# Kernel tuning notes

Measured on AMD Instinct MI355X. Metric: run time of the kernel, lower is better.

## Reference

```python
import jax, jax.numpy as jnp
import numpy as np

B, S, HID = 2, 1024, 2048
H, KV, D = 32, 8, 64          # heads, kv heads, head_dim
G = H // KV                    # GQA groups
THETA = 10000.0


def _rope_cos_sin(seq_len):
    # (S, D/2) cos/sin tables, interleaved-pair RoPE
    freqs = 1.0 / THETA ** (jnp.arange(0, D, 2, dtype=jnp.float32) / D)
    t = jnp.arange(seq_len, dtype=jnp.float32)
    f = jnp.outer(t, freqs)
    return jnp.cos(f), jnp.sin(f)


def _apply_rope(x, cos, sin):
    # x: (B, S, h, D); cos/sin: (S, D/2) -> broadcast (1, S, 1, D/2)
    c = cos[None, :, None, :]
    s = sin[None, :, None, :]
    xe, xo = x[..., ::2], x[..., 1::2]
    oe = xe * c - xo * s
    oo = xo * c + xe * s
    # re-interleave even/odd
    return jnp.stack([oe, oo], axis=-1).reshape(x.shape)


def setup_inputs() -> dict:
    key = jax.random.key(0)
    ks = jax.random.split(key, 5)
    return {
        "hidden_states": jax.random.normal(ks[0], (B, S, HID), jnp.float32),
        "Wq": jax.random.normal(ks[1], (HID, H * D), jnp.float32) * 0.02,
        "Wk": jax.random.normal(ks[2], (HID, KV * D), jnp.float32) * 0.02,
        "Wv": jax.random.normal(ks[3], (HID, KV * D), jnp.float32) * 0.02,
        "Wo": jax.random.normal(ks[4], (H * D, HID), jnp.float32) * 0.02,
    }


def reference(hidden_states, Wq, Wk, Wv, Wo):
    b, s, _ = hidden_states.shape
    q = (hidden_states @ Wq).reshape(b, s, H, D)
    k = (hidden_states @ Wk).reshape(b, s, KV, D)
    v = (hidden_states @ Wv).reshape(b, s, KV, D)

    cos, sin = _rope_cos_sin(s)
    q = _apply_rope(q, cos, sin)
    k = _apply_rope(k, cos, sin)

    # GQA: repeat kv heads to match query heads
    k = jnp.repeat(k, G, axis=2)  # (b, s, H, D)
    v = jnp.repeat(v, G, axis=2)

    scale = jnp.sqrt(jnp.float32(D))
    scores = jnp.einsum("bqhd,bkhd->bhqk", q, k) / scale  # (b, H, s, s)
    causal = jnp.tril(jnp.ones((s, s), jnp.float32))[None, None]
    scores = jnp.where(causal < 0.5, jnp.float32(-1e10), scores)
    weights = jax.nn.softmax(scores, axis=-1)
    ctx = jnp.einsum("bhqk,bkhd->bqhd", weights, v).reshape(b, s, H * D)
    return ctx @ Wo
```

## Files before the change

### kernel.cpp

```cpp
#include <hip/hip_runtime.h>
#include <hip/hip_bf16.h>

typedef __attribute__((ext_vector_type(8))) __bf16 bf16x8;
typedef __attribute__((ext_vector_type(4))) float f32x4;

#define MFMA16(a,b,c) __builtin_amdgcn_mfma_f32_16x16x32_bf16(a,b,c,0,0,0)

__device__ __forceinline__ unsigned short f2b(float x){
  __hip_bfloat16 h = __float2bfloat16(x);
  return __builtin_bit_cast(unsigned short, h);
}

__device__ __forceinline__ void gload16(const unsigned short* g, unsigned short* l){
  __builtin_amdgcn_global_load_lds(
      (const __attribute__((address_space(1))) unsigned int*)g,
      (__attribute__((address_space(3))) unsigned int*)l, 16, 0, 0);
}

__global__ void k_rope_table(float* __restrict__ ct, float* __restrict__ st){
  int i = blockIdx.x*256 + threadIdx.x;
  int t = i >> 5, f = i & 31;
  float freq = powf(10000.0f, -(float)f/32.0f);
  float a = (float)t * freq;
  ct[i] = cosf(a);
  st[i] = sinf(a);
}

__global__ void k_cvt(const float* __restrict__ src, unsigned short* __restrict__ dst, int n4){
  int i = blockIdx.x*256 + threadIdx.x;
  int stride = gridDim.x*256;
  for (; i < n4; i += stride){
    float4 v = ((const float4*)src)[i];
    ushort4 o; o.x=f2b(v.x); o.y=f2b(v.y); o.z=f2b(v.z); o.w=f2b(v.w);
    ((ushort4*)dst)[i] = o;
  }
}

__global__ __launch_bounds__(256) void k_prep_wt(
    const float* __restrict__ Wq, const float* __restrict__ Wk,
    const float* __restrict__ Wv, unsigned short* __restrict__ Wt){
  __shared__ float t[32][33];
  int n0 = blockIdx.x*32, k0 = blockIdx.y*32;
  const float* src; int N, nl;
  if (n0 < 2048)      { src=Wq; N=2048; nl=n0; }
  else if (n0 < 2560) { src=Wk; N=512;  nl=n0-2048; }
  else                { src=Wv; N=512;  nl=n0-2560; }
  int r = threadIdx.x>>5, c = threadIdx.x&31;
  #pragma unroll
  for (int it=0; it<4; ++it)
    t[r+8*it][c] = src[(size_t)(k0+r+8*it)*N + nl + c];
  __syncthreads();
  #pragma unroll
  for (int it=0; it<4; ++it)
    Wt[(size_t)(n0+r+8*it)*2048 + k0 + c] = f2b(t[c][r+8*it]);
}

__global__ __launch_bounds__(256) void k_prep_wo(
    const float* __restrict__ Wo, unsigned short* __restrict__ Wot){
  __shared__ float t[32][33];
  int n0 = blockIdx.x*32, k0 = blockIdx.y*32;
  int r = threadIdx.x>>5, c = threadIdx.x&31;
  #pragma unroll
  for (int it=0; it<4; ++it)
    t[r+8*it][c] = Wo[(size_t)(k0+r+8*it)*2048 + n0 + c];
  __syncthreads();
  #pragma unroll
  for (int it=0; it<4; ++it)
    Wot[(size_t)(n0+r+8*it)*2048 + k0 + c] = f2b(t[c][r+8*it]);
}

__global__ __launch_bounds__(256) void k_qkv(
    const unsigned short* __restrict__ A, const unsigned short* __restrict__ Bt,
    const float* __restrict__ ct, const float* __restrict__ st,
    unsigned short* __restrict__ qb, unsigned short* __restrict__ kb,
    unsigned short* __restrict__ vt)
{
  __shared__ unsigned short As[4][128*32];
  __shared__ unsigned short Bs[4][64*32];
  const int xcd = blockIdx.x & 7, idx = blockIdx.x >> 3;
  const int mt = idx & 15;
  const int nt = xcd*6 + (idx >> 4);
  const int bm = mt*128, bn_g = nt*64;
  const int tid=threadIdx.x, wave=tid>>6, lane=tid&63;
  const int lrow=lane&15, kgrp=lane>>4;
  const int wm=(wave>>1)*64, wn=(wave&1)*32;
  const int arow = tid>>2;
  const int acs  = (((tid&3) ^ ((tid>>3)&3)))*8;
  const int ksw  = (kgrp ^ ((lrow>>1)&3))*8;
  f32x4 acc[4][2] = {};

  #define STAGE_Q(buf, k0) do {                                                               \
    gload16(&A [(size_t)(bm + arow     )*2048 + (k0) + acs], &As[buf][(wave*64)*8]);          \
    gload16(&A [(size_t)(bm + 64 + arow)*2048 + (k0) + acs], &As[buf][(256 + wave*64)*8]);    \
    gload16(&Bt[(size_t)(bn_g + arow   )*2048 + (k0) + acs], &Bs[buf][(wave*64)*8]);          \
  } while(0)

  #define COMPUTE_Q(buf) do {                                          \
    bf16x8 a0,a1,a2,a3,b0,b1;                                          \
    a0 = *(const bf16x8*)&As[buf][(wm+ 0+lrow)*32 + ksw];              \
    a1 = *(const bf16x8*)&As[buf][(wm+16+lrow)*32 + ksw];              \
    a2 = *(const bf16x8*)&As[buf][(wm+32+lrow)*32 + ksw];              \
    a3 = *(const bf16x8*)&As[buf][(wm+48+lrow)*32 + ksw];              \
    b0 = *(const bf16x8*)&Bs[buf][(wn+ 0+lrow)*32 + ksw];              \
    b1 = *(const bf16x8*)&Bs[buf][(wn+16+lrow)*32 + ksw];              \
    acc[0][0]=MFMA16(a0,b0,acc[0][0]); acc[0][1]=MFMA16(a0,b1,acc[0][1]); \
    acc[1][0]=MFMA16(a1,b0,acc[1][0]); acc[1][1]=MFMA16(a1,b1,acc[1][1]); \
    acc[2][0]=MFMA16(a2,b0,acc[2][0]); acc[2][1]=MFMA16(a2,b1,acc[2][1]); \
    acc[3][0]=MFMA16(a3,b0,acc[3][0]); acc[3][1]=MFMA16(a3,b1,acc[3][1]); \
  } while(0)

  STAGE_Q(0, 0);
  STAGE_Q(1, 32);
  STAGE_Q(2, 64);
  #pragma unroll 1
  for (int t=0; t<64; ++t){
    asm volatile("s_waitcnt vmcnt(6)" ::: "memory");
    __builtin_amdgcn_s_barrier();
    int kn = t+3; if (kn > 63) kn = 63;
    STAGE_Q((t+3)&3, kn*32);
    COMPUTE_Q(t&3);
  }

  const int wtype = (bn_g < 2048) ? 0 : (bn_g < 2560 ? 1 : 2);
  const float qscale = 0.125f * 1.44269504f;
  #pragma unroll
  for (int mi=0;mi<4;mi++){
    #pragma unroll
    for (int ni=0;ni<2;ni++){
      int gr0 = bm + wm + mi*16 + kgrp*4;
      int gc  = bn_g + wn + ni*16 + lrow;
      if (wtype==2){
        int c = gc - 2560;
        int bq = gr0 >> 10, s0 = gr0 & 1023;
        ushort4 o;
        o.x=f2b(acc[mi][ni][0]); o.y=f2b(acc[mi][ni][1]);
        o.z=f2b(acc[mi][ni][2]); o.w=f2b(acc[mi][ni][3]);
        *(ushort4*)&vt[((size_t)(bq*512 + c))*1024 + s0] = o;
      } else {
        int d = gc & 63, fi = d >> 1, odd = d & 1;
        #pragma unroll
        for (int r=0;r<4;r++){
          float x = acc[mi][ni][r];
          float p = __shfl_xor(x, 1, 64);
          int srow = (gr0 + r) & 1023;
          float c = ct[srow*32 + fi], sn = st[srow*32 + fi];
          float o = odd ? (x*c + p*sn) : (x*c - p*sn);
          if (wtype==0) qb[(size_t)(gr0+r)*2048 + gc] = f2b(o*qscale);
          else          kb[(size_t)(gr0+r)*512 + (gc-2048)] = f2b(o);
        }
      }
    }
  }
  #undef STAGE_Q
  #undef COMPUTE_Q
}

#define LDP 72
__global__ __launch_bounds__(256) void k_attn(
    const unsigned short* __restrict__ qb, const unsigned short* __restrict__ kb,
    const unsigned short* __restrict__ vt, unsigned short* __restrict__ ctxb)
{
  __shared__ unsigned short Ks[2][64*LDP];
  __shared__ unsigned short Vs[2][64*LDP];
  __shared__ unsigned short QP[64*LDP];

  const int kvh = blockIdx.x & 7;
  const int s   = blockIdx.x >> 3;
  const int b   = s >> 5;
  const int hh  = (s >> 3) & 3;
  const int p   = s & 7;
  const int h   = kvh*4 + hh;

  const int tid=threadIdx.x, wave=tid>>6, lane=tid&63;
  const int lrow=lane&15, kgrp=lane>>4;
  const int wq = wave*16;
  const int sr = tid>>2, seg = (tid&3)*16;

  const unsigned short* kbase = kb + (size_t)(b*1024)*512 + kvh*64 + seg;
  const unsigned short* vbase = vt + ((size_t)(b*512 + kvh*64 + sr))*1024 + seg;

  #pragma unroll
  for (int phase=0; phase<2; ++phase){
    const int qt = phase==0 ? 15-p : p;
    const int q0 = qt*64;

    __syncthreads();
    {
      const unsigned short* src = qb + (size_t)(b*1024 + q0 + sr)*2048 + h*64 + seg;
      *(uint4*)&QP[sr*LDP + seg]     = *(const uint4*)&src[0];
      *(uint4*)&QP[sr*LDP + seg + 8] = *(const uint4*)&src[8];
      const unsigned short* ksrc = kbase + (size_t)sr*512;
      *(uint4*)&Ks[0][sr*LDP + seg]     = *(const uint4*)&ksrc[0];
      *(uint4*)&Ks[0][sr*LDP + seg + 8] = *(const uint4*)&ksrc[8];
      *(uint4*)&Vs[0][sr*LDP + seg]     = *(const uint4*)&vbase[0];
      *(uint4*)&Vs[0][sr*LDP + seg + 8] = *(const uint4*)&vbase[8];
    }
    __syncthreads();

    bf16x8 qa[2];
    #pragma unroll
    for (int ks=0;ks<2;ks++)
      qa[ks] = *(const bf16x8*)&QP[(wq+lrow)*LDP + ks*32 + kgrp*8];

    float m_run = -1e30f, l_run = 0.f;
    f32x4 out[4] = {};

    for (int j=0;j<=qt;j++){
      const int cb = j&1;
      uint4 kra, krb, vra, vrb;
      if (j < qt){
        const unsigned short* ksrc = kbase + (size_t)((j+1)*64 + sr)*512;
        kra = *(const uint4*)&ksrc[0]; krb = *(const uint4*)&ksrc[8];
        const unsigned short* vsrc = vbase + (j+1)*64;
        vra = *(const uint4*)&vsrc[0]; vrb = *(const uint4*)&vsrc[8];
      }

      f32x4 sc[4] = {};
      __builtin_amdgcn_s_setprio(1);
      #pragma unroll
      for (int ks=0;ks<2;ks++){
        #pragma unroll
        for (int ni=0;ni<4;ni++){
          bf16x8 kf = *(const bf16x8*)&Ks[cb][(ni*16+lrow)*LDP + ks*32 + kgrp*8];
          sc[ni] = MFMA16(kf, qa[ks], sc[ni]);
        }
      }
      __builtin_amdgcn_s_setprio(0);

      if (j == qt){
        #pragma unroll
        for (int ni=0;ni<4;ni++)
          #pragma unroll
          for (int r=0;r<4;r++)
            if (ni*16 + kgrp*4 + r > wq + lrow) sc[ni][r] = -1e30f;
      }

      float mx = sc[0][0];
      #pragma unroll
      for (int ni=0;ni<4;ni++)
        #pragma unroll
        for (int r=0;r<4;r++) mx = fmaxf(mx, sc[ni][r]);
      mx = fmaxf(mx, __shfl_xor(mx, 16, 64));
      mx = fmaxf(mx, __shfl_xor(mx, 32, 64));
      if (__any(mx > m_run + 12.0f)){
        float mnew = fmaxf(m_run, mx);
        float corr = exp2f(m_run - mnew);
        m_run = mnew;
        l_run *= corr;
        #pragma unroll
        for (int di=0;di<4;di++)
          #pragma unroll
          for (int r=0;r<4;r++) out[di][r] *= corr;
      }
      float rsum = 0.f;
      #pragma unroll
      for (int ni=0;ni<4;ni++)
        #pragma unroll
        for (int r=0;r<4;r++){
          float pv = exp2f(sc[ni][r] - m_run);
          sc[ni][r] = pv;
          rsum += pv;
        }
      rsum += __shfl_xor(rsum, 16, 64);
      rsum += __shfl_xor(rsum, 32, 64);
      l_run += rsum;

      #pragma unroll
      for (int ni=0;ni<4;ni++){
        ushort4 o;
        o.x=f2b(sc[ni][0]); o.y=f2b(sc[ni][1]);
        o.z=f2b(sc[ni][2]); o.w=f2b(sc[ni][3]);
        *(ushort4*)&QP[(wq+lrow)*LDP + ni*16 + kgrp*4] = o;
      }

      __builtin_amdgcn_s_setprio(1);
      #pragma unroll
      for (int ks2=0;ks2<2;ks2++){
        bf16x8 pb = *(const bf16x8*)&QP[(wq+lrow)*LDP + ks2*32 + kgrp*8];
        #pragma unroll
        for (int di=0;di<4;di++){
          bf16x8 vf = *(const bf16x8*)&Vs[cb][(di*16+lrow)*LDP + ks2*32 + kgrp*8];
          out[di] = MFMA16(vf, pb, out[di]);
        }
      }
      __builtin_amdgcn_s_setprio(0);

      if (j < qt){
        const int nb = (j+1)&1;
        *(uint4*)&Ks[nb][sr*LDP + seg]     = kra;
        *(uint4*)&Ks[nb][sr*LDP + seg + 8] = krb;
        *(uint4*)&Vs[nb][sr*LDP + seg]     = vra;
        *(uint4*)&Vs[nb][sr*LDP + seg + 8] = vrb;
      }
      __syncthreads();
    }

    float rl = 1.0f / l_run;
    #pragma unroll
    for (int di=0;di<4;di++){
      ushort4 o;
      o.x=f2b(out[di][0]*rl); o.y=f2b(out[di][1]*rl);
      o.z=f2b(out[di][2]*rl); o.w=f2b(out[di][3]*rl);
      *(ushort4*)&ctxb[(size_t)(b*1024 + q0 + wq + lrow)*2048
                       + h*64 + di*16 + kgrp*4] = o;
    }
  }
}

__global__ __launch_bounds__(256) void k_oproj(
    const unsigned short* __restrict__ A, const unsigned short* __restrict__ Bt,
    float* __restrict__ out)
{
  __shared__ unsigned short As[4][128*32];
  __shared__ unsigned short Bs[4][64*32];
  const int xcd = blockIdx.x & 7, idx = blockIdx.x >> 3;
  const int mt = idx & 15;
  const int nt = xcd*4 + (idx >> 4);
  const int bm = mt*128, bn = nt*64;
  const int tid=threadIdx.x, wave=tid>>6, lane=tid&63;
  const int lrow=lane&15, kgrp=lane>>4;
  const int wm=(wave>>1)*64, wn=(wave&1)*32;
  const int arow = tid>>2;
  const int acs  = (((tid&3) ^ ((tid>>3)&3)))*8;
  const int ksw  = (kgrp ^ ((lrow>>1)&3))*8;
  f32x4 acc[4][2] = {};

  #define STAGE_O(buf, k0) do {                                                               \
    gload16(&A [(size_t)(bm + arow     )*2048 + (k0) + acs], &As[buf][(wave*64)*8]);          \
    gload16(&A [(size_t)(bm + 64 + arow)*2048 + (k0) + acs], &As[buf][(256 + wave*64)*8]);    \
    gload16(&Bt[(size_t)(bn + arow     )*2048 + (k0) + acs], &Bs[buf][(wave*64)*8]);          \
  } while(0)

  #define COMPUTE_O(buf) do {                                          \
    bf16x8 a0,a1,a2,a3,b0,b1;                                          \
    a0 = *(const bf16x8*)&As[buf][(wm+ 0+lrow)*32 + ksw];              \
    a1 = *(const bf16x8*)&As[buf][(wm+16+lrow)*32 + ksw];              \
    a2 = *(const bf16x8*)&As[buf][(wm+32+lrow)*32 + ksw];              \
    a3 = *(const bf16x8*)&As[buf][(wm+48+lrow)*32 + ksw];              \
    b0 = *(const bf16x8*)&Bs[buf][(wn+ 0+lrow)*32 + ksw];              \
    b1 = *(const bf16x8*)&Bs[buf][(wn+16+lrow)*32 + ksw];              \
    acc[0][0]=MFMA16(a0,b0,acc[0][0]); acc[0][1]=MFMA16(a0,b1,acc[0][1]); \
    acc[1][0]=MFMA16(a1,b0,acc[1][0]); acc[1][1]=MFMA16(a1,b1,acc[1][1]); \
    acc[2][0]=MFMA16(a2,b0,acc[2][0]); acc[2][1]=MFMA16(a2,b1,acc[2][1]); \
    acc[3][0]=MFMA16(a3,b0,acc[3][0]); acc[3][1]=MFMA16(a3,b1,acc[3][1]); \
  } while(0)

  STAGE_O(0, 0);
  STAGE_O(1, 32);
  STAGE_O(2, 64);
  #pragma unroll 1
  for (int t=0; t<64; ++t){
    asm volatile("s_waitcnt vmcnt(6)" ::: "memory");
    __builtin_amdgcn_s_barrier();
    int kn = t+3; if (kn > 63) kn = 63;
    STAGE_O((t+3)&3, kn*32);
    COMPUTE_O(t&3);
  }

  #pragma unroll
  for (int mi=0;mi<4;mi++)
    #pragma unroll
    for (int ni=0;ni<2;ni++){
      int gr0 = bm + wm + mi*16 + kgrp*4;
      int gc  = bn + wn + ni*16 + lrow;
      #pragma unroll
      for (int r=0;r<4;r++)
        out[(size_t)(gr0+r)*2048 + gc] = acc[mi][ni][r];
    }
  #undef STAGE_O
  #undef COMPUTE_O
}

extern "C" void kernel_launch(void* const* d_in, const int* in_sizes, int n_in,
                              void* d_out, int out_size, void* d_ws, size_t ws_size,
                              hipStream_t stream)
{
  const float* X  = (const float*)d_in[0];
  const float* Wq = (const float*)d_in[1];
  const float* Wk = (const float*)d_in[2];
  const float* Wv = (const float*)d_in[3];
  const float* Wo = (const float*)d_in[4];
  float* out = (float*)d_out;
  char* ws = (char*)d_ws;

  const size_t MB = 1048576;
  float* ct = (float*)ws;
  float* st = (float*)(ws + 128*1024);
  unsigned short* Xb   = (unsigned short*)(ws + 256*1024);
  unsigned short* Wt   = (unsigned short*)(ws + 256*1024 + 8*MB);
  unsigned short* Wot  = (unsigned short*)(ws + 256*1024 + 20*MB);
  unsigned short* qb   = (unsigned short*)(ws + 256*1024 + 28*MB);
  unsigned short* kb   = (unsigned short*)(ws + 256*1024 + 36*MB);
  unsigned short* vt   = (unsigned short*)(ws + 256*1024 + 38*MB);
  unsigned short* ctxb = (unsigned short*)(ws + 256*1024 + 40*MB);

  hipLaunchKernelGGL(k_rope_table, dim3(128), dim3(256), 0, stream, ct, st);
  hipLaunchKernelGGL(k_cvt, dim3(2048), dim3(256), 0, stream, X, Xb, 2048*2048/4);
  hipLaunchKernelGGL(k_prep_wt, dim3(96,64), dim3(256), 0, stream, Wq, Wk, Wv, Wt);
  hipLaunchKernelGGL(k_prep_wo, dim3(64,64), dim3(256), 0, stream, Wo, Wot);
  hipLaunchKernelGGL(k_qkv, dim3(768), dim3(256), 0, stream,
                     Xb, Wt, ct, st, qb, kb, vt);
  hipLaunchKernelGGL(k_attn, dim3(512), dim3(256), 0, stream, qb, kb, vt, ctxb);
  hipLaunchKernelGGL(k_oproj, dim3(512), dim3(256), 0, stream, ctxb, Wot, out);
}
```

Baseline: 145.4 us.

## Merge prep kernels into one launch and use triple-buffered GEMM pipelines

Four preprocessing kernels (RoPE table, X conversion, QKV weight transpose, Wo transpose) become a single kernel that dispatches on block index, cutting three launches and the gaps between them. The QKV and output-projection GEMMs drop from four LDS stages to three, prefetching two tiles ahead instead of three. The smaller LDS footprint may allow more resident blocks per CU, at the cost of less latency hiding for global loads.

```diff
diff --git a/kernel.cpp b/kernel.cpp
--- a/kernel.cpp
+++ b/kernel.cpp
@@ -17,56 +17,64 @@
       (__attribute__((address_space(3))) unsigned int*)l, 16, 0, 0);
 }
 
-__global__ void k_rope_table(float* __restrict__ ct, float* __restrict__ st){
-  int i = blockIdx.x*256 + threadIdx.x;
-  int t = i >> 5, f = i & 31;
-  float freq = powf(10000.0f, -(float)f/32.0f);
-  float a = (float)t * freq;
-  ct[i] = cosf(a);
-  st[i] = sinf(a);
-}
-
-__global__ void k_cvt(const float* __restrict__ src, unsigned short* __restrict__ dst, int n4){
-  int i = blockIdx.x*256 + threadIdx.x;
-  int stride = gridDim.x*256;
-  for (; i < n4; i += stride){
-    float4 v = ((const float4*)src)[i];
-    ushort4 o; o.x=f2b(v.x); o.y=f2b(v.y); o.z=f2b(v.z); o.w=f2b(v.w);
-    ((ushort4*)dst)[i] = o;
-  }
-}
-
-__global__ __launch_bounds__(256) void k_prep_wt(
-    const float* __restrict__ Wq, const float* __restrict__ Wk,
-    const float* __restrict__ Wv, unsigned short* __restrict__ Wt){
+__global__ __launch_bounds__(256) void k_prep(
+    const float* __restrict__ X,  const float* __restrict__ Wq,
+    const float* __restrict__ Wk, const float* __restrict__ Wv,
+    const float* __restrict__ Wo,
+    float* __restrict__ ct, float* __restrict__ st,
+    unsigned short* __restrict__ Xb, unsigned short* __restrict__ Wt,
+    unsigned short* __restrict__ Wot)
+{
   __shared__ float t[32][33];
-  int n0 = blockIdx.x*32, k0 = blockIdx.y*32;
-  const float* src; int N, nl;
-  if (n0 < 2048)      { src=Wq; N=2048; nl=n0; }
-  else if (n0 < 2560) { src=Wk; N=512;  nl=n0-2048; }
-  else                { src=Wv; N=512;  nl=n0-2560; }
-  int r = threadIdx.x>>5, c = threadIdx.x&31;
-  #pragma unroll
-  for (int it=0; it<4; ++it)
-    t[r+8*it][c] = src[(size_t)(k0+r+8*it)*N + nl + c];
-  __syncthreads();
-  #pragma unroll
-  for (int it=0; it<4; ++it)
-    Wt[(size_t)(n0+r+8*it)*2048 + k0 + c] = f2b(t[c][r+8*it]);
-}
-
-__global__ __launch_bounds__(256) void k_prep_wo(
-    const float* __restrict__ Wo, unsigned short* __restrict__ Wot){
-  __shared__ float t[32][33];
-  int n0 = blockIdx.x*32, k0 = blockIdx.y*32;
-  int r = threadIdx.x>>5, c = threadIdx.x&31;
-  #pragma unroll
-  for (int it=0; it<4; ++it)
-    t[r+8*it][c] = Wo[(size_t)(k0+r+8*it)*2048 + n0 + c];
-  __syncthreads();
-  #pragma unroll
-  for (int it=0; it<4; ++it)
-    Wot[(size_t)(n0+r+8*it)*2048 + k0 + c] = f2b(t[c][r+8*it]);
+  int bid = blockIdx.x;
+  if (bid < 128){
+    int i = bid*256 + threadIdx.x;
+    int tt = i >> 5, f = i & 31;
+    float freq = powf(10000.0f, -(float)f/32.0f);
+    float a = (float)tt * freq;
+    ct[i] = cosf(a); st[i] = sinf(a);
+    return;
+  }
+  bid -= 128;
+  if (bid < 1024){
+    const int n4 = 2048*2048/4;
+    for (int i = bid*256 + threadIdx.x; i < n4; i += 1024*256){
+      float4 v = ((const float4*)X)[i];
+      ushort4 o; o.x=f2b(v.x); o.y=f2b(v.y); o.z=f2b(v.z); o.w=f2b(v.w);
+      ((ushort4*)Xb)[i] = o;
+    }
+    return;
+  }
+  bid -= 1024;
+  if (bid < 6144){
+    int bx = bid % 96, by = bid / 96;
+    int n0 = bx*32, k0 = by*32;
+    const float* src; int N, nl;
+    if (n0 < 2048)      { src=Wq; N=2048; nl=n0; }
+    else if (n0 < 2560) { src=Wk; N=512;  nl=n0-2048; }
+    else                { src=Wv; N=512;  nl=n0-2560; }
+    int r = threadIdx.x>>5, c = threadIdx.x&31;
+    #pragma unroll
+    for (int it=0; it<4; ++it)
+      t[r+8*it][c] = src[(size_t)(k0+r+8*it)*N + nl + c];
+    __syncthreads();
+    #pragma unroll
+    for (int it=0; it<4; ++it)
+      Wt[(size_t)(n0+r+8*it)*2048 + k0 + c] = f2b(t[c][r+8*it]);
+    return;
+  }
+  bid -= 6144;
+  {
+    int n0 = (bid & 63)*32, k0 = (bid >> 6)*32;
+    int r = threadIdx.x>>5, c = threadIdx.x&31;
+    #pragma unroll
+    for (int it=0; it<4; ++it)
+      t[r+8*it][c] = Wo[(size_t)(k0+r+8*it)*2048 + n0 + c];
+    __syncthreads();
+    #pragma unroll
+    for (int it=0; it<4; ++it)
+      Wot[(size_t)(n0+r+8*it)*2048 + k0 + c] = f2b(t[c][r+8*it]);
+  }
 }
 
 __global__ __launch_bounds__(256) void k_qkv(
@@ -75,8 +83,8 @@
     unsigned short* __restrict__ qb, unsigned short* __restrict__ kb,
     unsigned short* __restrict__ vt)
 {
-  __shared__ unsigned short As[4][128*32];
-  __shared__ unsigned short Bs[4][64*32];
+  __shared__ unsigned short As[3][128*32];
+  __shared__ unsigned short Bs[3][64*32];
   const int xcd = blockIdx.x & 7, idx = blockIdx.x >> 3;
   const int mt = idx & 15;
   const int nt = xcd*6 + (idx >> 4);
@@ -111,14 +119,16 @@
 
   STAGE_Q(0, 0);
   STAGE_Q(1, 32);
-  STAGE_Q(2, 64);
+  int cur = 0;
   #pragma unroll 1
   for (int t=0; t<64; ++t){
-    asm volatile("s_waitcnt vmcnt(6)" ::: "memory");
+    asm volatile("s_waitcnt vmcnt(3)" ::: "memory");
     __builtin_amdgcn_s_barrier();
-    int kn = t+3; if (kn > 63) kn = 63;
-    STAGE_Q((t+3)&3, kn*32);
-    COMPUTE_Q(t&3);
+    int kn = t+2; if (kn > 63) kn = 63;
+    int nb = cur+2; if (nb > 2) nb -= 3;
+    STAGE_Q(nb, kn*32);
+    COMPUTE_Q(cur);
+    cur = (cur==2) ? 0 : cur+1;
   }
 
   const int wtype = (bn_g < 2048) ? 0 : (bn_g < 2560 ? 1 : 2);
@@ -311,8 +321,8 @@
     const unsigned short* __restrict__ A, const unsigned short* __restrict__ Bt,
     float* __restrict__ out)
 {
-  __shared__ unsigned short As[4][128*32];
-  __shared__ unsigned short Bs[4][64*32];
+  __shared__ unsigned short As[3][128*32];
+  __shared__ unsigned short Bs[3][64*32];
   const int xcd = blockIdx.x & 7, idx = blockIdx.x >> 3;
   const int mt = idx & 15;
   const int nt = xcd*4 + (idx >> 4);
@@ -347,14 +357,16 @@
 
   STAGE_O(0, 0);
   STAGE_O(1, 32);
-  STAGE_O(2, 64);
+  int cur = 0;
   #pragma unroll 1
   for (int t=0; t<64; ++t){
-    asm volatile("s_waitcnt vmcnt(6)" ::: "memory");
+    asm volatile("s_waitcnt vmcnt(3)" ::: "memory");
     __builtin_amdgcn_s_barrier();
-    int kn = t+3; if (kn > 63) kn = 63;
-    STAGE_O((t+3)&3, kn*32);
-    COMPUTE_O(t&3);
+    int kn = t+2; if (kn > 63) kn = 63;
+    int nb = cur+2; if (nb > 2) nb -= 3;
+    STAGE_O(nb, kn*32);
+    COMPUTE_O(cur);
+    cur = (cur==2) ? 0 : cur+1;
   }
 
   #pragma unroll
@@ -394,10 +406,8 @@
   unsigned short* vt   = (unsigned short*)(ws + 256*1024 + 38*MB);
   unsigned short* ctxb = (unsigned short*)(ws + 256*1024 + 40*MB);
 
-  hipLaunchKernelGGL(k_rope_table, dim3(128), dim3(256), 0, stream, ct, st);
-  hipLaunchKernelGGL(k_cvt, dim3(2048), dim3(256), 0, stream, X, Xb, 2048*2048/4);
-  hipLaunchKernelGGL(k_prep_wt, dim3(96,64), dim3(256), 0, stream, Wq, Wk, Wv, Wt);
-  hipLaunchKernelGGL(k_prep_wo, dim3(64,64), dim3(256), 0, stream, Wo, Wot);
+  hipLaunchKernelGGL(k_prep, dim3(11392), dim3(256), 0, stream,
+                     X, Wq, Wk, Wv, Wo, ct, st, Xb, Wt, Wot);
   hipLaunchKernelGGL(k_qkv, dim3(768), dim3(256), 0, stream,
                      Xb, Wt, ct, st, qb, kb, vt);
   hipLaunchKernelGGL(k_attn, dim3(512), dim3(256), 0, stream, qb, kb, vt, ctxb);
```

New measurement: 132.2 us. -9.0%, faster.
